# Kernel optimization log

Measured on AMD Instinct MI355X. Metric: run time of the kernel, lower is better.

## Reference

```python
import jax, jax.numpy as jnp
import numpy as np

N, E = 50000, 800000
F_IN, EDGE_DIM, H, C = 128, 64, 8, 32
NEG_SLOPE = 0.2


def setup_inputs() -> dict:
    key = jax.random.key(0)
    ks = jax.random.split(key, 9)
    return {
        "x": jax.random.normal(ks[0], (N, F_IN), dtype=jnp.float32),
        "edge_index": jax.random.randint(ks[1], (2, E), 0, N, dtype=jnp.int32),
        "edge_attr": jax.random.normal(ks[2], (E, EDGE_DIM), dtype=jnp.float32),
        "W": jax.random.normal(ks[3], (F_IN, H * C), dtype=jnp.float32) * 0.05,
        "att_src": jax.random.normal(ks[4], (H, C), dtype=jnp.float32) * 0.05,
        "att_dst": jax.random.normal(ks[5], (H, C), dtype=jnp.float32) * 0.05,
        "W_edge": jax.random.normal(ks[6], (EDGE_DIM, H * C), dtype=jnp.float32) * 0.05,
        "att_edge": jax.random.normal(ks[7], (H, C), dtype=jnp.float32) * 0.05,
        "bias": jax.random.normal(ks[8], (H * C,), dtype=jnp.float32) * 0.05,
    }


def reference(x, edge_index, edge_attr, W, att_src, att_dst, W_edge, att_edge, bias):
    src, dst = edge_index[0], edge_index[1]  # messages flow src -> dst
    # Pre-activation ReLU from Graph_intra.forward
    xr = jax.nn.relu(x)
    # Linear projection, per-head view: [N, H, C]
    xs = (xr @ W).reshape(N, H, C)
    # Per-node attention logits: [N, H]
    a_src = jnp.einsum("nhc,hc->nh", xs, att_src)
    a_dst = jnp.einsum("nhc,hc->nh", xs, att_dst)
    # Edge-feature attention contribution: [E, H]
    e_proj = (edge_attr @ W_edge).reshape(E, H, C)
    a_edge = jnp.einsum("ehc,hc->eh", e_proj, att_edge)
    # Per-edge logits + LeakyReLU
    alpha = jax.nn.leaky_relu(a_src[src] + a_dst[dst] + a_edge, NEG_SLOPE)  # [E, H]
    # Segment softmax over destination neighborhoods
    seg_max = jax.ops.segment_max(alpha, dst, num_segments=N)
    seg_max = jnp.where(jnp.isfinite(seg_max), seg_max, 0.0)
    alpha = jnp.exp(alpha - seg_max[dst])
    seg_sum = jax.ops.segment_sum(alpha, dst, num_segments=N)
    alpha = alpha / (seg_sum[dst] + 1e-16)
    # Weighted message aggregation: scatter-add alpha_e * x_src[e]
    msgs = alpha[:, :, None] * xs[src]  # [E, H, C]
    out = jax.ops.segment_sum(msgs, dst, num_segments=N)  # [N, H, C]
    return out.reshape(N, H * C) + bias
```

## Files before the change

### kernel.cpp

```cpp
#include <hip/hip_runtime.h>

#define N_NODES 50000
#define E_EDGES 800000
#define F_IN    128
#define EDGE_DIM 64
#define HC      256
#define NEG_SLOPE 0.2f

typedef __attribute__((ext_vector_type(8))) short short8;
typedef __attribute__((ext_vector_type(4))) float f32x4;

__device__ __forceinline__ unsigned short f2bf(float f) {
    unsigned u = __builtin_bit_cast(unsigned, f);
    u += 0x7fffu + ((u >> 16) & 1u);
    return (unsigned short)(u >> 16);
}
__device__ __forceinline__ float bf2f(unsigned short b) {
    return __builtin_bit_cast(float, (unsigned)b << 16);
}

__global__ __launch_bounds__(256) void k_pre(const float* __restrict__ W,
        const float* __restrict__ att_src, const float* __restrict__ att_dst,
        const float* __restrict__ W_edge, const float* __restrict__ att_edge,
        unsigned short* __restrict__ W_T, unsigned short* __restrict__ WaT,
        unsigned short* __restrict__ WaE, int* __restrict__ counts, int* __restrict__ gcur) {
    int idx = blockIdx.x * 256 + threadIdx.x;
    if (idx < N_NODES) counts[idx] = 0;
    if (idx == 0) *gcur = 0;
    if (idx < 32768) {
        int n = idx >> 7, k = idx & 127;
        W_T[n * 128 + k] = f2bf(W[k * 256 + n]);
    }
    if (idx < 2048) {
        int col = idx & 15, k = idx >> 4;
        const float* att = (col < 8) ? att_src : att_dst;
        int h = col & 7;
        float s = 0.f;
        #pragma unroll
        for (int c = 0; c < 32; ++c)
            s = fmaf(W[k * 256 + h * 32 + c], att[h * 32 + c], s);
        WaT[col * 128 + k] = f2bf(s);
    }
    if (idx < 1024) {
        int c = idx >> 6, k = idx & 63;
        float s = 0.f;
        if (c < 8) {
            #pragma unroll
            for (int cc = 0; cc < 32; ++cc)
                s = fmaf(W_edge[k * 256 + c * 32 + cc], att_edge[c * 32 + cc], s);
        }
        WaE[c * 64 + k] = (c < 8) ? f2bf(s) : (unsigned short)0;
    }
}

#define HIST_BLOCKS 782
#define ALOG_BLOCKS 782
__global__ __launch_bounds__(256) void kA(const float* __restrict__ x,
        const unsigned short* __restrict__ WaT,
        const int4* __restrict__ dst4, int* __restrict__ counts, int4* __restrict__ slot4,
        float* __restrict__ a_src, float* __restrict__ a_dst) {
    int t = threadIdx.x;
    if (blockIdx.x < HIST_BLOCKS) {
        int i = blockIdx.x * 256 + t;
        if (i < E_EDGES / 4) {
            int4 d = dst4[i];
            int4 sl;
            sl.x = atomicAdd(&counts[d.x], 1);
            sl.y = atomicAdd(&counts[d.y], 1);
            sl.z = atomicAdd(&counts[d.z], 1);
            sl.w = atomicAdd(&counts[d.w], 1);
            slot4[i] = sl;
        }
        return;
    }
    int tile = (blockIdx.x - HIST_BLOCKS) * 4 + (t >> 6);
    if (tile >= N_NODES / 16) return;
    int lane = t & 63, mr = lane & 15, g = lane >> 4;
    int node = tile * 16 + mr;
    f32x4 acc = (f32x4){0.f, 0.f, 0.f, 0.f};
    #pragma unroll
    for (int ks = 0; ks < 4; ++ks) {
        const float* xp = &x[(size_t)node * 128 + ks * 32 + g * 8];
        short8 a;
        #pragma unroll
        for (int j = 0; j < 8; ++j) a[j] = (short)f2bf(fmaxf(xp[j], 0.f));
        short8 b = *(const short8*)&WaT[mr * 128 + ks * 32 + g * 8];
        acc = __builtin_amdgcn_mfma_f32_16x16x32_bf16(a, b, acc, 0, 0, 0);
    }
    #pragma unroll
    for (int r = 0; r < 4; ++r) {
        int n2 = tile * 16 + g * 4 + r;
        if (mr < 8) a_src[n2 * 8 + mr]       = acc[r];
        else        a_dst[n2 * 8 + (mr - 8)] = acc[r];
    }
}

__global__ __launch_bounds__(256) void kB_alloc(const int* __restrict__ counts,
                                                int* __restrict__ starts,
                                                int* __restrict__ gcur) {
    int n = blockIdx.x * 256 + threadIdx.x;
    int c = (n < N_NODES) ? counts[n] : 0;
    int incl = c;
    #pragma unroll
    for (int off = 1; off < 64; off <<= 1) {
        int u = __shfl_up(incl, off);
        if ((threadIdx.x & 63) >= off) incl += u;
    }
    int total = __shfl(incl, 63);
    int wavebase = 0;
    if ((threadIdx.x & 63) == 63) wavebase = atomicAdd(gcur, total);
    wavebase = __shfl(wavebase, 63);
    if (n < N_NODES) starts[n] = wavebase + incl - c;
}

__global__ __launch_bounds__(256) void kB2(const int* __restrict__ dst,
        const int* __restrict__ slot, const int* __restrict__ starts,
        const int* __restrict__ src, int* __restrict__ pos, int* __restrict__ src_perm) {
    int e = blockIdx.x * 1024 + threadIdx.x;
    #pragma unroll
    for (int i = 0; i < 4; ++i, e += 256) {
        if (e < E_EDGES) {
            int p = starts[dst[e]] + slot[e];
            pos[e] = p;
            src_perm[p] = src[e];
        }
    }
}

#define NT_TILES 782
#define GEMM_BLOCKS 512
__global__ __launch_bounds__(256) void kC(const float* __restrict__ x,
        const unsigned short* __restrict__ W_T, const unsigned short* __restrict__ WaE,
        const float* __restrict__ ea,
        const int* __restrict__ src, const int* __restrict__ pos,
        const float* __restrict__ a_src, const float* __restrict__ a_dst,
        const int* __restrict__ dst,
        unsigned short* __restrict__ xs, _Float16* __restrict__ w_perm) {
    __shared__ __align__(16) char smem[32768];
    int t = threadIdx.x;

    if (blockIdx.x >= GEMM_BLOCKS) {
        int* s_sn  = (int*)smem;
        int* s_dn  = (int*)(smem + 1024);
        int* s_pos = (int*)(smem + 2048);
        _Float16* s_w = (_Float16*)(smem + 3072);
        int blockbase = (blockIdx.x - GEMM_BLOCKS) * 256;
        {
            int e = blockbase + t;
            s_sn[t] = src[e];
            s_dn[t] = dst[e];
            s_pos[t] = pos[e];
        }
        __syncthreads();
        int lane = t & 63, w = t >> 6;
        int mr = lane & 15, g = lane >> 4;
        short8 b0 = *(const short8*)&WaE[mr * 64 + g * 8];
        short8 b1 = *(const short8*)&WaE[mr * 64 + 32 + g * 8];
        #pragma unroll
        for (int ti = 0; ti < 4; ++ti) {
            int lb = w * 64 + ti * 16;
            int er = blockbase + lb + mr;
            const float* ap = &ea[(size_t)er * 64 + g * 8];
            short8 a0, a1;
            #pragma unroll
            for (int j = 0; j < 8; ++j) a0[j] = (short)f2bf(ap[j]);
            #pragma unroll
            for (int j = 0; j < 8; ++j) a1[j] = (short)f2bf(ap[32 + j]);
            f32x4 acc = (f32x4){0.f, 0.f, 0.f, 0.f};
            acc = __builtin_amdgcn_mfma_f32_16x16x32_bf16(a0, b0, acc, 0, 0, 0);
            acc = __builtin_amdgcn_mfma_f32_16x16x32_bf16(a1, b1, acc, 0, 0, 0);
            if (mr < 8) {
                #pragma unroll
                for (int r = 0; r < 4; ++r) {
                    int le = lb + g * 4 + r;
                    int sn = s_sn[le], dn = s_dn[le];
                    float v = acc[r] + a_src[sn * 8 + mr] + a_dst[dn * 8 + mr];
                    v = (v > 0.f) ? v : NEG_SLOPE * v;
                    s_w[le * 8 + mr] = (_Float16)__expf(v);
                }
            }
        }
        __syncthreads();
        *(int4*)&w_perm[(size_t)s_pos[t] * 8] = *(const int4*)&s_w[t * 8];
        return;
    }

    unsigned short* sB = (unsigned short*)smem;
    int ch = blockIdx.x >> 8;
    int rt0 = blockIdx.x & 255;
    for (int G = t; G < 2048; G += 256) {
        int nn = G >> 4, gi = G & 15;
        *(int4*)&sB[(nn * 16 + (gi ^ (nn & 7))) * 8] =
            *(const int4*)&W_T[(ch * 128 + nn) * 128 + gi * 8];
    }
    __syncthreads();
    int lane = t & 63, w = t >> 6, mr = lane & 15, g = lane >> 4;

    for (int rt = rt0; rt < NT_TILES; rt += 256) {
        int node = rt * 64 + w * 16 + mr;
        short8 a[4];
        if (node < N_NODES) {
            #pragma unroll
            for (int ks = 0; ks < 4; ++ks) {
                const float* xp = &x[(size_t)node * 128 + ks * 32 + g * 8];
                #pragma unroll
                for (int j = 0; j < 8; ++j) a[ks][j] = (short)f2bf(fmaxf(xp[j], 0.f));
            }
        } else {
            #pragma unroll
            for (int ks = 0; ks < 4; ++ks)
                #pragma unroll
                for (int j = 0; j < 8; ++j) a[ks][j] = 0;
        }

        f32x4 acc[8];
        #pragma unroll
        for (int i = 0; i < 8; ++i) acc[i] = (f32x4){0.f, 0.f, 0.f, 0.f};

        #pragma unroll
        for (int ks = 0; ks < 4; ++ks) {
            int posk = (ks * 4 + g) ^ (mr & 7);
            #pragma unroll
            for (int nt = 0; nt < 8; ++nt) {
                short8 b = *(const short8*)&sB[((nt * 16 + mr) * 16 + posk) * 8];
                acc[nt] = __builtin_amdgcn_mfma_f32_16x16x32_bf16(a[ks], b, acc[nt], 0, 0, 0);
            }
        }

        #pragma unroll
        for (int r = 0; r < 4; ++r) {
            int node2 = rt * 64 + w * 16 + g * 4 + r;
            if (node2 < N_NODES) {
                #pragma unroll
                for (int nt = 0; nt < 8; ++nt)
                    xs[(size_t)node2 * 256 + ch * 128 + nt * 16 + mr] = f2bf(acc[nt][r]);
            }
        }
    }
}

__global__ __launch_bounds__(256) void k6_wave(
    const int* __restrict__ starts, const int* __restrict__ counts,
    const _Float16* __restrict__ w_perm, const int* __restrict__ src_perm,
    const unsigned short* __restrict__ xs, const float* __restrict__ bias,
    float* __restrict__ out) {
    int lane = threadIdx.x & 63;
    int n = blockIdx.x * 4 + (threadIdx.x >> 6);
    if (n >= N_NODES) return;
    int start = starts[n], cnt = counts[n];
    int j = lane >> 3;
    int l5 = lane & 31;
    int h2 = lane >> 5;
    int hq = l5 >> 2;

    float acc[8];
    #pragma unroll
    for (int k = 0; k < 8; ++k) acc[k] = 0.f;
    float psum = 0.f;

    for (int base = 0; base < cnt; base += 8) {
        int nk = cnt - base; if (nk > 8) nk = 8;
        float wv = (float)w_perm[(size_t)(start + base) * 8 + lane];
        if (j >= nk) wv = 0.f;
        psum += wv;
        int sv = src_perm[start + base + (lane & 7)];
        #pragma unroll
        for (int jj = 0; jj < 8; jj += 2) {
            int eidx = jj + h2;
            int s = __shfl(sv, eidx);
            s = (eidx < nk) ? s : 0;
            float w = __shfl(wv, eidx * 8 + hq);
            int4 xv = *(const int4*)&xs[(size_t)s * 256 + l5 * 8];
            acc[0] = fmaf(w, bf2f((unsigned short)(xv.x & 0xffff)), acc[0]);
            acc[1] = fmaf(w, bf2f((unsigned short)((unsigned)xv.x >> 16)), acc[1]);
            acc[2] = fmaf(w, bf2f((unsigned short)(xv.y & 0xffff)), acc[2]);
            acc[3] = fmaf(w, bf2f((unsigned short)((unsigned)xv.y >> 16)), acc[3]);
            acc[4] = fmaf(w, bf2f((unsigned short)(xv.z & 0xffff)), acc[4]);
            acc[5] = fmaf(w, bf2f((unsigned short)((unsigned)xv.z >> 16)), acc[5]);
            acc[6] = fmaf(w, bf2f((unsigned short)(xv.w & 0xffff)), acc[6]);
            acc[7] = fmaf(w, bf2f((unsigned short)((unsigned)xv.w >> 16)), acc[7]);
        }
    }
    #pragma unroll
    for (int k = 0; k < 8; ++k) acc[k] += __shfl_xor(acc[k], 32);
    psum += __shfl_xor(psum, 8);
    psum += __shfl_xor(psum, 16);
    psum += __shfl_xor(psum, 32);
    float denom = __shfl(psum, hq);
    float rinv = 1.0f / (denom + 1e-16f);

    if (h2 == 0) {
        const float* bp = &bias[l5 * 8];
        f32x4 o0, o1;
        #pragma unroll
        for (int k = 0; k < 4; ++k) o0[k] = acc[k] * rinv + bp[k];
        #pragma unroll
        for (int k = 0; k < 4; ++k) o1[k] = acc[4 + k] * rinv + bp[4 + k];
        float* op = &out[(size_t)n * 256 + l5 * 8];
        __builtin_nontemporal_store(o0, (f32x4*)op);
        __builtin_nontemporal_store(o1, (f32x4*)(op + 4));
    }
}

extern "C" void kernel_launch(void* const* d_in, const int* in_sizes, int n_in,
                              void* d_out, int out_size, void* d_ws, size_t ws_size,
                              hipStream_t stream) {
    const float* x         = (const float*)d_in[0];
    const int*   ei        = (const int*)d_in[1];
    const float* edge_attr = (const float*)d_in[2];
    const float* W         = (const float*)d_in[3];
    const float* att_src   = (const float*)d_in[4];
    const float* att_dst   = (const float*)d_in[5];
    const float* W_edge    = (const float*)d_in[6];
    const float* att_edge  = (const float*)d_in[7];
    const float* bias      = (const float*)d_in[8];
    float* out = (float*)d_out;

    const int* e_src = ei;
    const int* e_dst = ei + E_EDGES;

    char* p = (char*)d_ws;
    unsigned short* xs = (unsigned short*)p; p += (size_t)N_NODES * HC * 2;
    float* a_src   = (float*)p; p += (size_t)N_NODES * 8 * 4;
    float* a_dst   = (float*)p; p += (size_t)N_NODES * 8 * 4;
    _Float16* w_perm = (_Float16*)p; p += (size_t)E_EDGES * 8 * 2 + 256;
    int* src_perm  = (int*)p;   p += (size_t)E_EDGES * 4 + 256;
    int* slot      = (int*)p;   p += (size_t)E_EDGES * 4 + 256;
    int* pos       = (int*)p;   p += (size_t)E_EDGES * 4 + 256;
    unsigned short* W_T  = (unsigned short*)p; p += 32768 * 2;
    unsigned short* WaT  = (unsigned short*)p; p += 2048 * 2;
    unsigned short* WaE  = (unsigned short*)p; p += 1024 * 2;
    int* counts    = (int*)p;   p += 200192;
    int* starts    = (int*)p;   p += 200192;
    int* gcur      = (int*)p;   p += 256;

    hipLaunchKernelGGL(k_pre, dim3(196), dim3(256), 0, stream,
                       W, att_src, att_dst, W_edge, att_edge, W_T, WaT, WaE, counts, gcur);
    hipLaunchKernelGGL(kA, dim3(HIST_BLOCKS + ALOG_BLOCKS), dim3(256), 0, stream,
                       x, WaT, (const int4*)e_dst, counts, (int4*)slot, a_src, a_dst);
    hipLaunchKernelGGL(kB_alloc, dim3(196), dim3(256), 0, stream,
                       counts, starts, gcur);
    hipLaunchKernelGGL(kB2, dim3((E_EDGES + 1023) / 1024), dim3(256), 0, stream,
                       e_dst, slot, starts, e_src, pos, src_perm);
    hipLaunchKernelGGL(kC, dim3(GEMM_BLOCKS + E_EDGES / 256), dim3(256), 0, stream,
                       x, W_T, WaE, edge_attr, e_src, pos, a_src, a_dst, e_dst,
                       xs, w_perm);
    hipLaunchKernelGGL(k6_wave, dim3(N_NODES / 4), dim3(256), 0, stream,
                       starts, counts, w_perm, src_perm, xs, bias, out);
}
```

Measured before the change: 211.4 us.

## Move node GEMM into histogram kernel and fuse CSR scatter into edge kernel

The xs projection GEMM moves into the first kernel, running alongside the dst histogram and attention-logit blocks. The position and src_perm scatter formerly done in kB2 is folded into the edge-logit kernel, which computes pos inline. This removes one launch and the pos array round-trip through global memory. In exchange the first kernel carries 32 KB of shared memory for every block, which may lower occupancy for the histogram blocks.

After: 210.2 us. Within noise of the previous version (-0.6%).

```diff
diff --git a/kernel.cpp b/kernel.cpp
--- a/kernel.cpp
+++ b/kernel.cpp
@@ -53,45 +53,105 @@
     }
 }
 
+#define NT_TILES 782
+#define GEMM_BLOCKS 512
 #define HIST_BLOCKS 782
 #define ALOG_BLOCKS 782
-__global__ __launch_bounds__(256) void kA(const float* __restrict__ x,
-        const unsigned short* __restrict__ WaT,
+__global__ __launch_bounds__(256) void kBig(const float* __restrict__ x,
+        const unsigned short* __restrict__ W_T, const unsigned short* __restrict__ WaT,
         const int4* __restrict__ dst4, int* __restrict__ counts, int4* __restrict__ slot4,
-        float* __restrict__ a_src, float* __restrict__ a_dst) {
+        unsigned short* __restrict__ xs, float* __restrict__ a_src, float* __restrict__ a_dst) {
+    __shared__ __align__(16) unsigned short sB[128 * 128];
     int t = threadIdx.x;
-    if (blockIdx.x < HIST_BLOCKS) {
-        int i = blockIdx.x * 256 + t;
-        if (i < E_EDGES / 4) {
-            int4 d = dst4[i];
-            int4 sl;
-            sl.x = atomicAdd(&counts[d.x], 1);
-            sl.y = atomicAdd(&counts[d.y], 1);
-            sl.z = atomicAdd(&counts[d.z], 1);
-            sl.w = atomicAdd(&counts[d.w], 1);
-            slot4[i] = sl;
+
+    if (blockIdx.x >= GEMM_BLOCKS) {
+        int part = blockIdx.x - GEMM_BLOCKS;
+        if (part < HIST_BLOCKS) {
+            int i = part * 256 + t;
+            if (i < E_EDGES / 4) {
+                int4 d = dst4[i];
+                int4 sl;
+                sl.x = atomicAdd(&counts[d.x], 1);
+                sl.y = atomicAdd(&counts[d.y], 1);
+                sl.z = atomicAdd(&counts[d.z], 1);
+                sl.w = atomicAdd(&counts[d.w], 1);
+                slot4[i] = sl;
+            }
+            return;
+        }
+        int tile = (part - HIST_BLOCKS) * 4 + (t >> 6);
+        if (tile >= N_NODES / 16) return;
+        int lane = t & 63, mr = lane & 15, g = lane >> 4;
+        int node = tile * 16 + mr;
+        f32x4 acc = (f32x4){0.f, 0.f, 0.f, 0.f};
+        #pragma unroll
+        for (int ks = 0; ks < 4; ++ks) {
+            const float* xp = &x[(size_t)node * 128 + ks * 32 + g * 8];
+            short8 a;
+            #pragma unroll
+            for (int j = 0; j < 8; ++j) a[j] = (short)f2bf(fmaxf(xp[j], 0.f));
+            short8 b = *(const short8*)&WaT[mr * 128 + ks * 32 + g * 8];
+            acc = __builtin_amdgcn_mfma_f32_16x16x32_bf16(a, b, acc, 0, 0, 0);
+        }
+        #pragma unroll
+        for (int r = 0; r < 4; ++r) {
+            int n2 = tile * 16 + g * 4 + r;
+            if (mr < 8) a_src[n2 * 8 + mr]       = acc[r];
+            else        a_dst[n2 * 8 + (mr - 8)] = acc[r];
         }
         return;
     }
-    int tile = (blockIdx.x - HIST_BLOCKS) * 4 + (t >> 6);
-    if (tile >= N_NODES / 16) return;
-    int lane = t & 63, mr = lane & 15, g = lane >> 4;
-    int node = tile * 16 + mr;
-    f32x4 acc = (f32x4){0.f, 0.f, 0.f, 0.f};
-    #pragma unroll
-    for (int ks = 0; ks < 4; ++ks) {
-        const float* xp = &x[(size_t)node * 128 + ks * 32 + g * 8];
-        short8 a;
-        #pragma unroll
-        for (int j = 0; j < 8; ++j) a[j] = (short)f2bf(fmaxf(xp[j], 0.f));
-        short8 b = *(const short8*)&WaT[mr * 128 + ks * 32 + g * 8];
-        acc = __builtin_amdgcn_mfma_f32_16x16x32_bf16(a, b, acc, 0, 0, 0);
-    }
-    #pragma unroll
-    for (int r = 0; r < 4; ++r) {
-        int n2 = tile * 16 + g * 4 + r;
-        if (mr < 8) a_src[n2 * 8 + mr]       = acc[r];
-        else        a_dst[n2 * 8 + (mr - 8)] = acc[r];
+
+    int ch = blockIdx.x >> 8;
+    int rt0 = blockIdx.x & 255;
+    for (int G = t; G < 2048; G += 256) {
+        int nn = G >> 4, gi = G & 15;
+        *(int4*)&sB[(nn * 16 + (gi ^ (nn & 7))) * 8] =
+            *(const int4*)&W_T[(ch * 128 + nn) * 128 + gi * 8];
+    }
+    __syncthreads();
+    int lane = t & 63, w = t >> 6, mr = lane & 15, g = lane >> 4;
+
+    for (int rt = rt0; rt < NT_TILES; rt += 256) {
+        int node = rt * 64 + w * 16 + mr;
+        short8 a[4];
+        if (node < N_NODES) {
+            #pragma unroll
+            for (int ks = 0; ks < 4; ++ks) {
+                const float* xp = &x[(size_t)node * 128 + ks * 32 + g * 8];
+                #pragma unroll
+                for (int j = 0; j < 8; ++j) a[ks][j] = (short)f2bf(fmaxf(xp[j], 0.f));
+            }
+        } else {
+            #pragma unroll
+            for (int ks = 0; ks < 4; ++ks)
+                #pragma unroll
+                for (int j = 0; j < 8; ++j) a[ks][j] = 0;
+        }
+
+        f32x4 acc[8];
+        #pragma unroll
+        for (int i = 0; i < 8; ++i) acc[i] = (f32x4){0.f, 0.f, 0.f, 0.f};
+
+        #pragma unroll
+        for (int ks = 0; ks < 4; ++ks) {
+            int posk = (ks * 4 + g) ^ (mr & 7);
+            #pragma unroll
+            for (int nt = 0; nt < 8; ++nt) {
+                short8 b = *(const short8*)&sB[((nt * 16 + mr) * 16 + posk) * 8];
+                acc[nt] = __builtin_amdgcn_mfma_f32_16x16x32_bf16(a[ks], b, acc[nt], 0, 0, 0);
+            }
+        }
+
+        #pragma unroll
+        for (int r = 0; r < 4; ++r) {
+            int node2 = rt * 64 + w * 16 + g * 4 + r;
+            if (node2 < N_NODES) {
+                #pragma unroll
+                for (int nt = 0; nt < 8; ++nt)
+                    xs[(size_t)node2 * 256 + ch * 128 + nt * 16 + mr] = f2bf(acc[nt][r]);
+            }
+        }
     }
 }
 
@@ -113,130 +173,54 @@
     if (n < N_NODES) starts[n] = wavebase + incl - c;
 }
 
-__global__ __launch_bounds__(256) void kB2(const int* __restrict__ dst,
+__global__ __launch_bounds__(256) void kEdge(const float* __restrict__ ea,
+        const unsigned short* __restrict__ WaE,
+        const int* __restrict__ src, const int* __restrict__ dst,
         const int* __restrict__ slot, const int* __restrict__ starts,
-        const int* __restrict__ src, int* __restrict__ pos, int* __restrict__ src_perm) {
-    int e = blockIdx.x * 1024 + threadIdx.x;
+        const float* __restrict__ a_src, const float* __restrict__ a_dst,
+        _Float16* __restrict__ w_perm, int* __restrict__ src_perm) {
+    __shared__ int s_sn[256], s_dn[256], s_pos[256];
+    __shared__ _Float16 s_w[256 * 8];
+    int t = threadIdx.x;
+    int blockbase = blockIdx.x * 256;
+    {
+        int e = blockbase + t;
+        int dn = dst[e], sn = src[e];
+        int pos = starts[dn] + slot[e];
+        s_sn[t] = sn; s_dn[t] = dn; s_pos[t] = pos;
+        src_perm[pos] = sn;
+    }
+    __syncthreads();
+    int lane = t & 63, w = t >> 6;
+    int mr = lane & 15, g = lane >> 4;
+    short8 b0 = *(const short8*)&WaE[mr * 64 + g * 8];
+    short8 b1 = *(const short8*)&WaE[mr * 64 + 32 + g * 8];
     #pragma unroll
-    for (int i = 0; i < 4; ++i, e += 256) {
-        if (e < E_EDGES) {
-            int p = starts[dst[e]] + slot[e];
-            pos[e] = p;
-            src_perm[p] = src[e];
-        }
-    }
-}
-
-#define NT_TILES 782
-#define GEMM_BLOCKS 512
-__global__ __launch_bounds__(256) void kC(const float* __restrict__ x,
-        const unsigned short* __restrict__ W_T, const unsigned short* __restrict__ WaE,
-        const float* __restrict__ ea,
-        const int* __restrict__ src, const int* __restrict__ pos,
-        const float* __restrict__ a_src, const float* __restrict__ a_dst,
-        const int* __restrict__ dst,
-        unsigned short* __restrict__ xs, _Float16* __restrict__ w_perm) {
-    __shared__ __align__(16) char smem[32768];
-    int t = threadIdx.x;
-
-    if (blockIdx.x >= GEMM_BLOCKS) {
-        int* s_sn  = (int*)smem;
-        int* s_dn  = (int*)(smem + 1024);
-        int* s_pos = (int*)(smem + 2048);
-        _Float16* s_w = (_Float16*)(smem + 3072);
-        int blockbase = (blockIdx.x - GEMM_BLOCKS) * 256;
-        {
-            int e = blockbase + t;
-            s_sn[t] = src[e];
-            s_dn[t] = dst[e];
-            s_pos[t] = pos[e];
-        }
-        __syncthreads();
-        int lane = t & 63, w = t >> 6;
-        int mr = lane & 15, g = lane >> 4;
-        short8 b0 = *(const short8*)&WaE[mr * 64 + g * 8];
-        short8 b1 = *(const short8*)&WaE[mr * 64 + 32 + g * 8];
-        #pragma unroll
-        for (int ti = 0; ti < 4; ++ti) {
-            int lb = w * 64 + ti * 16;
-            int er = blockbase + lb + mr;
-            const float* ap = &ea[(size_t)er * 64 + g * 8];
-            short8 a0, a1;
-            #pragma unroll
-            for (int j = 0; j < 8; ++j) a0[j] = (short)f2bf(ap[j]);
-            #pragma unroll
-            for (int j = 0; j < 8; ++j) a1[j] = (short)f2bf(ap[32 + j]);
-            f32x4 acc = (f32x4){0.f, 0.f, 0.f, 0.f};
-            acc = __builtin_amdgcn_mfma_f32_16x16x32_bf16(a0, b0, acc, 0, 0, 0);
-            acc = __builtin_amdgcn_mfma_f32_16x16x32_bf16(a1, b1, acc, 0, 0, 0);
-            if (mr < 8) {
-                #pragma unroll
-                for (int r = 0; r < 4; ++r) {
-                    int le = lb + g * 4 + r;
-                    int sn = s_sn[le], dn = s_dn[le];
-                    float v = acc[r] + a_src[sn * 8 + mr] + a_dst[dn * 8 + mr];
-                    v = (v > 0.f) ? v : NEG_SLOPE * v;
-                    s_w[le * 8 + mr] = (_Float16)__expf(v);
-                }
-            }
-        }
-        __syncthreads();
-        *(int4*)&w_perm[(size_t)s_pos[t] * 8] = *(const int4*)&s_w[t * 8];
-        return;
-    }
-
-    unsigned short* sB = (unsigned short*)smem;
-    int ch = blockIdx.x >> 8;
-    int rt0 = blockIdx.x & 255;
-    for (int G = t; G < 2048; G += 256) {
-        int nn = G >> 4, gi = G & 15;
-        *(int4*)&sB[(nn * 16 + (gi ^ (nn & 7))) * 8] =
-            *(const int4*)&W_T[(ch * 128 + nn) * 128 + gi * 8];
+    for (int ti = 0; ti < 4; ++ti) {
+        int lb = w * 64 + ti * 16;
+        int er = blockbase + lb + mr;
+        const float* ap = &ea[(size_t)er * 64 + g * 8];
+        short8 a0, a1;
+        #pragma unroll
+        for (int j = 0; j < 8; ++j) a0[j] = (short)f2bf(ap[j]);
+        #pragma unroll
+        for (int j = 0; j < 8; ++j) a1[j] = (short)f2bf(ap[32 + j]);
+        f32x4 acc = (f32x4){0.f, 0.f, 0.f, 0.f};
+        acc = __builtin_amdgcn_mfma_f32_16x16x32_bf16(a0, b0, acc, 0, 0, 0);
+        acc = __builtin_amdgcn_mfma_f32_16x16x32_bf16(a1, b1, acc, 0, 0, 0);
+        if (mr < 8) {
+            #pragma unroll
+            for (int r = 0; r < 4; ++r) {
+                int le = lb + g * 4 + r;
+                int sn = s_sn[le], dn = s_dn[le];
+                float v = acc[r] + a_src[sn * 8 + mr] + a_dst[dn * 8 + mr];
+                v = (v > 0.f) ? v : NEG_SLOPE * v;
+                s_w[le * 8 + mr] = (_Float16)__expf(v);
+            }
+        }
     }
     __syncthreads();
-    int lane = t & 63, w = t >> 6, mr = lane & 15, g = lane >> 4;
-
-    for (int rt = rt0; rt < NT_TILES; rt += 256) {
-        int node = rt * 64 + w * 16 + mr;
-        short8 a[4];
-        if (node < N_NODES) {
-            #pragma unroll
-            for (int ks = 0; ks < 4; ++ks) {
-                const float* xp = &x[(size_t)node * 128 + ks * 32 + g * 8];
-                #pragma unroll
-                for (int j = 0; j < 8; ++j) a[ks][j] = (short)f2bf(fmaxf(xp[j], 0.f));
-            }
-        } else {
-            #pragma unroll
-            for (int ks = 0; ks < 4; ++ks)
-                #pragma unroll
-                for (int j = 0; j < 8; ++j) a[ks][j] = 0;
-        }
-
-        f32x4 acc[8];
-        #pragma unroll
-        for (int i = 0; i < 8; ++i) acc[i] = (f32x4){0.f, 0.f, 0.f, 0.f};
-
-        #pragma unroll
-        for (int ks = 0; ks < 4; ++ks) {
-            int posk = (ks * 4 + g) ^ (mr & 7);
-            #pragma unroll
-            for (int nt = 0; nt < 8; ++nt) {
-                short8 b = *(const short8*)&sB[((nt * 16 + mr) * 16 + posk) * 8];
-                acc[nt] = __builtin_amdgcn_mfma_f32_16x16x32_bf16(a[ks], b, acc[nt], 0, 0, 0);
-            }
-        }
-
-        #pragma unroll
-        for (int r = 0; r < 4; ++r) {
-            int node2 = rt * 64 + w * 16 + g * 4 + r;
-            if (node2 < N_NODES) {
-                #pragma unroll
-                for (int nt = 0; nt < 8; ++nt)
-                    xs[(size_t)node2 * 256 + ch * 128 + nt * 16 + mr] = f2bf(acc[nt][r]);
-            }
-        }
-    }
+    *(int4*)&w_perm[(size_t)s_pos[t] * 8] = *(const int4*)&s_w[t * 8];
 }
 
 __global__ __launch_bounds__(256) void k6_wave(
@@ -326,7 +310,6 @@
     _Float16* w_perm = (_Float16*)p; p += (size_t)E_EDGES * 8 * 2 + 256;
     int* src_perm  = (int*)p;   p += (size_t)E_EDGES * 4 + 256;
     int* slot      = (int*)p;   p += (size_t)E_EDGES * 4 + 256;
-    int* pos       = (int*)p;   p += (size_t)E_EDGES * 4 + 256;
     unsigned short* W_T  = (unsigned short*)p; p += 32768 * 2;
     unsigned short* WaT  = (unsigned short*)p; p += 2048 * 2;
     unsigned short* WaE  = (unsigned short*)p; p += 1024 * 2;
@@ -336,15 +319,13 @@
 
     hipLaunchKernelGGL(k_pre, dim3(196), dim3(256), 0, stream,
                        W, att_src, att_dst, W_edge, att_edge, W_T, WaT, WaE, counts, gcur);
-    hipLaunchKernelGGL(kA, dim3(HIST_BLOCKS + ALOG_BLOCKS), dim3(256), 0, stream,
-                       x, WaT, (const int4*)e_dst, counts, (int4*)slot, a_src, a_dst);
+    hipLaunchKernelGGL(kBig, dim3(GEMM_BLOCKS + HIST_BLOCKS + ALOG_BLOCKS), dim3(256), 0, stream,
+                       x, W_T, WaT, (const int4*)e_dst, counts, (int4*)slot, xs, a_src, a_dst);
     hipLaunchKernelGGL(kB_alloc, dim3(196), dim3(256), 0, stream,
                        counts, starts, gcur);
-    hipLaunchKernelGGL(kB2, dim3((E_EDGES + 1023) / 1024), dim3(256), 0, stream,
-                       e_dst, slot, starts, e_src, pos, src_perm);
-    hipLaunchKernelGGL(kC, dim3(GEMM_BLOCKS + E_EDGES / 256), dim3(256), 0, stream,
-                       x, W_T, WaE, edge_attr, e_src, pos, a_src, a_dst, e_dst,
-                       xs, w_perm);
+    hipLaunchKernelGGL(kEdge, dim3(E_EDGES / 256), dim3(256), 0, stream,
+                       edge_attr, WaE, e_src, e_dst, slot, starts,
+                       a_src, a_dst, w_perm, src_perm);
     hipLaunchKernelGGL(k6_wave, dim3(N_NODES / 4), dim3(256), 0, stream,
                        starts, counts, w_perm, src_perm, xs, bias, out);
 }
```
